# Kernel tuning notes

Hardware: AMD Instinct MI355X
Metric: run time of the kernel (lower is better)

Reference implementation:

```python
import jax, jax.numpy as jnp
import numpy as np

B, D, Q, K, C = 1024, 256, 131072, 200, 1000
TEMPERATURE = 0.07  # train-mode temperature (test=False path)
EPS = 1e-05


def setup_inputs() -> dict:
    key = jax.random.key(0)
    k1, k2, k3 = jax.random.split(key, 3)
    x = jax.random.normal(k1, (B, D), dtype=jnp.float32)
    memory = jax.random.normal(k2, (Q, D), dtype=jnp.float32)
    memory_label = jax.random.randint(k3, (Q,), 0, C, dtype=jnp.int64 if jax.config.jax_enable_x64 else jnp.int32)
    return {"x": x, "memory": memory, "memory_label": memory_label}


def reference(x, memory, memory_label):
    # dist = normalize(x) @ memory.T  -> [B, Q]
    xn = x / jnp.linalg.norm(x, axis=-1, keepdims=True)
    dist = jnp.einsum('bd,qd->bq', xn, memory)
    # top-k similarities and indices -> [B, K]
    sim_weight, sim_indices = jax.lax.top_k(dist, K)
    sim_labels = memory_label[sim_indices]  # [B, K]
    w = jax.nn.softmax(sim_weight / TEMPERATURE, axis=1)  # [B, K]
    # Fused one-hot scatter + weighted sum: scatter-add weights per class.
    rows = jnp.arange(B)[:, None]  # [B, 1] broadcast against [B, K]
    pred_scores = jnp.zeros((B, C), dtype=w.dtype).at[rows, sim_labels].add(w)
    return jnp.minimum(pred_scores + EPS, 1.0)
```

## Files before the change

### kernel.cpp

```cpp
#include <hip/hip_runtime.h>
#include <hip/hip_bf16.h>
#include <hip/hip_fp16.h>

#define B_ 1024
#define D_ 256
#define Q_ 131072
#define K_ 200
#define C_ 1000
#define INV_T 14.285714285714286f
#define EPS_ 1e-5f
#define CAP 2048
#define T0S 43.2f

#define TBM 128
#define NSL 16
#define HCAP 1024
#define FT 512

typedef __attribute__((ext_vector_type(2))) long lng2;
typedef __attribute__((ext_vector_type(4))) float f32x4;

__device__ __forceinline__ unsigned key_of(float v) {
    unsigned u = __float_as_uint(v);
    return (u & 0x80000000u) ? ~u : (u | 0x80000000u);
}
__device__ __forceinline__ int binof(float v) {
    int b = (int)(key_of(v) >> 16) - 0xC000;
    return b < 0 ? 0 : (b > 255 ? 255 : b);
}
__device__ __forceinline__ unsigned pk4(float a, float b, float c, float d) {
    int u = __builtin_amdgcn_cvt_pk_fp8_f32(a, b, 0, false);
    u = __builtin_amdgcn_cvt_pk_fp8_f32(c, d, u, true);
    return (unsigned)u;
}

#define MFMA_FP8 __builtin_amdgcn_mfma_f32_16x16x32_fp8_fp8

__global__ __launch_bounds__(256) void normsplit_kernel(const float* __restrict__ x,
                                                        float* __restrict__ xn,
                                                        unsigned char* __restrict__ af8,
                                                        unsigned* __restrict__ cnt) {
    int row = blockIdx.x, tid = threadIdx.x;
    if (tid == 0) cnt[row] = 0u;
    float v = x[row * D_ + tid];
    float s = v * v;
#pragma unroll
    for (int off = 32; off > 0; off >>= 1) s += __shfl_xor(s, off);
    __shared__ float wsum[4];
    int lane = tid & 63, wid = tid >> 6;
    if (lane == 0) wsum[wid] = s;
    __syncthreads();
    float tot = wsum[0] + wsum[1] + wsum[2] + wsum[3];
    float xv = v / sqrtf(tot);
    xn[row * D_ + tid] = xv;
    int t = tid >> 5, kb = (tid >> 3) & 3, j = tid & 7;
    int p = __builtin_amdgcn_cvt_pk_fp8_f32(xv * 16.f, 0.f, 0, false);
    af8[row * 256 + kb * 64 + t * 8 + j] = (unsigned char)(p & 0xFF);
}

__global__ __launch_bounds__(256) void convB_kernel(const float* __restrict__ m,
                                                    uint4* __restrict__ bf8,
                                                    __half* __restrict__ mh) {
    const int NCH = Q_ * D_ / 16;
    for (int g = blockIdx.x * 256 + threadIdx.x; g < NCH; g += gridDim.x * 256) {
        int panel = g >> 9, o = g & 511;
        int P = o >> 7, r = o & 127, ch = r >> 6, w = r & 63, kb = w >> 4, c = w & 15;
        int q = panel * 32 + ch * 16 + c;
        const float* src = m + (size_t)q * D_ + P * 64 + kb * 8;
        float4 f0 = *(const float4*)(src);
        float4 f1 = *(const float4*)(src + 4);
        float4 g0 = *(const float4*)(src + 32);
        float4 g1 = *(const float4*)(src + 36);
        uint4 ov;
        ov.x = pk4(f0.x, f0.y, f0.z, f0.w);
        ov.y = pk4(f1.x, f1.y, f1.z, f1.w);
        ov.z = pk4(g0.x, g0.y, g0.z, g0.w);
        ov.w = pk4(g1.x, g1.y, g1.z, g1.w);
        bf8[g] = ov;
        __half* mhp = mh + (size_t)q * D_ + P * 64 + kb * 8;
        __half2 ph[4];
        ph[0] = __floats2half2_rn(f0.x, f0.y); ph[1] = __floats2half2_rn(f0.z, f0.w);
        ph[2] = __floats2half2_rn(f1.x, f1.y); ph[3] = __floats2half2_rn(f1.z, f1.w);
        *(uint4*)mhp = *(const uint4*)ph;
        ph[0] = __floats2half2_rn(g0.x, g0.y); ph[1] = __floats2half2_rn(g0.z, g0.w);
        ph[2] = __floats2half2_rn(g1.x, g1.y); ph[3] = __floats2half2_rn(g1.z, g1.w);
        *(uint4*)(mhp + 32) = *(const uint4*)ph;
    }
}

__global__ __launch_bounds__(512, 4) void mfma_gemm_filter(const unsigned char* __restrict__ Af8,
                                                           const unsigned char* __restrict__ Bf8,
                                                           unsigned* __restrict__ candi,
                                                           unsigned* __restrict__ cnt) {
    __shared__ unsigned hits[HCAP];
    __shared__ unsigned hcnt;

    const int tid = threadIdx.x;
    const int lane = tid & 63, wid = tid >> 6;
    const int wr = wid >> 2, wn = wid & 3;
    const int l15 = lane & 15, kb = lane >> 4;

    const int l = blockIdx.x;
    const int logical = (l & 7) * 128 + (l >> 3);
    const int cg = logical >> 3;
    const int band = logical & 7;
    const int arow0 = band * TBM;

    if (tid == 0) hcnt = 0u;
    __syncthreads();

    long a[4][8];
#pragma unroll
    for (int m = 0; m < 4; ++m) {
        const unsigned char* ab = Af8 + (size_t)(arow0 + wr * 64 + m * 16 + l15) * 256 + kb * 64;
#pragma unroll
        for (int t2 = 0; t2 < 4; ++t2) {
            lng2 v = *(const lng2*)(ab + t2 * 16);
            a[m][2 * t2] = v.x;
            a[m][2 * t2 + 1] = v.y;
        }
    }

    const unsigned char* Bwave = Bf8 + (size_t)cg * 262144 + (wn >> 1) * 8192
                               + (wn & 1) * 1024 + (((kb << 4) + l15) << 4) + 4096;
    const unsigned char* pA = Bwave;
    const unsigned char* pB = Bwave + 16384;
#define LDBo(PTR, P_) (*(const lng2*)((PTR) + ((P_) * 2048 - 4096)))
#define LOADSL(BUF, PTR) do {                                                  \
    BUF[0] = LDBo(PTR, 0); BUF[1] = LDBo(PTR, 1);                              \
    BUF[2] = LDBo(PTR, 2); BUF[3] = LDBo(PTR, 3);                              \
} while (0)

    f32x4 zero4 = {0.f, 0.f, 0.f, 0.f};
    f32x4 acc[4];

#define MF4Z(AK, BV) do {                                                      \
    acc[0] = MFMA_FP8(a[0][AK], (BV), zero4, 0, 0, 0);                         \
    acc[1] = MFMA_FP8(a[1][AK], (BV), zero4, 0, 0, 0);                         \
    acc[2] = MFMA_FP8(a[2][AK], (BV), zero4, 0, 0, 0);                         \
    acc[3] = MFMA_FP8(a[3][AK], (BV), zero4, 0, 0, 0);                         \
} while (0)
#define MF4(AK, BV) do {                                                       \
    acc[0] = MFMA_FP8(a[0][AK], (BV), acc[0], 0, 0, 0);                        \
    acc[1] = MFMA_FP8(a[1][AK], (BV), acc[1], 0, 0, 0);                        \
    acc[2] = MFMA_FP8(a[2][AK], (BV), acc[2], 0, 0, 0);                        \
    acc[3] = MFMA_FP8(a[3][AK], (BV), acc[3], 0, 0, 0);                        \
} while (0)
#define COMPSL(BUF) do {                                                       \
    __builtin_amdgcn_s_setprio(1);                                             \
    MF4Z(0, BUF[0].x); MF4(1, BUF[0].y);                                       \
    MF4(2, BUF[1].x);  MF4(3, BUF[1].y);                                       \
    MF4(4, BUF[2].x);  MF4(5, BUF[2].y);                                       \
    MF4(6, BUF[3].x);  MF4(7, BUF[3].y);                                       \
    __builtin_amdgcn_s_setprio(0);                                             \
} while (0)

#define FILTER(I_) do {                                                        \
    float mx0 = fmaxf(fmaxf(acc[0][0], acc[0][1]), fmaxf(acc[0][2], acc[0][3])); \
    float mx1 = fmaxf(fmaxf(acc[1][0], acc[1][1]), fmaxf(acc[1][2], acc[1][3])); \
    float mx2 = fmaxf(fmaxf(acc[2][0], acc[2][1]), fmaxf(acc[2][2], acc[2][3])); \
    float mx3 = fmaxf(fmaxf(acc[3][0], acc[3][1]), fmaxf(acc[3][2], acc[3][3])); \
    if (fmaxf(fmaxf(mx0, mx1), fmaxf(mx2, mx3)) > T0S) {                       \
        const unsigned gc_ = (unsigned)(cg * 1024 + (wn + 4 * (I_)) * 16 + l15); \
        _Pragma("unroll")                                                      \
        for (int m = 0; m < 4; ++m)                                            \
            _Pragma("unroll")                                                  \
            for (int r = 0; r < 4; ++r)                                        \
                if (acc[m][r] > T0S) {                                         \
                    unsigned lr_ = (unsigned)(wr * 64 + m * 16 + kb * 4 + r);  \
                    unsigned p_ = atomicAdd(&hcnt, 1u);                        \
                    if (p_ < HCAP) hits[p_] = (lr_ << 17) | gc_;               \
                }                                                              \
    }                                                                          \
} while (0)

    lng2 bufA[4], bufB[4];
    LOADSL(bufA, pA);
#pragma unroll 1
    for (int i2 = 0; i2 < NSL; i2 += 2) {
        LOADSL(bufB, pB);
        pB += 32768;
        COMPSL(bufA);
        FILTER(i2);
        if (i2 + 2 < NSL) { pA += 32768; LOADSL(bufA, pA); }
        COMPSL(bufB);
        FILTER(i2 + 1);
    }

    __syncthreads();
    const unsigned nh = (hcnt < (unsigned)HCAP) ? hcnt : (unsigned)HCAP;
    for (unsigned i = tid; i < nh; i += 512) {
        unsigned e = hits[i];
        int grow = band * TBM + (int)(e >> 17);
        unsigned gcol = e & 0x1FFFFu;
        unsigned pos = atomicAdd(&cnt[grow], 1u);
        if (pos < CAP) candi[(long long)grow * CAP + pos] = gcol;
    }
#undef LDBo
#undef LOADSL
#undef MF4Z
#undef MF4
#undef COMPSL
#undef FILTER
}

__global__ __launch_bounds__(FT) void final_kernel(const unsigned* __restrict__ cnt,
                                                   const unsigned* __restrict__ candi,
                                                   const float* __restrict__ xn,
                                                   const __half* __restrict__ mh,
                                                   const int* __restrict__ labels,
                                                   float* __restrict__ out) {
    __shared__ float cval[CAP];
    __shared__ unsigned cidx[CAP];
    __shared__ unsigned char incl[CAP];
    __shared__ float xs[D_];
    __shared__ float bins[C_];
    __shared__ float segf[FT];
    __shared__ unsigned hist[256];
    __shared__ float binval[256];
    __shared__ int binpos[256];
    __shared__ int sh_bstar, sh_g0, sh_m;

    const int tid = threadIdx.x;
    const int row = blockIdx.x;
    unsigned c = cnt[row];
    const int n = (c < (unsigned)CAP) ? (int)c : CAP;

    if (tid < D_) xs[tid] = xn[row * D_ + tid];
    for (int i = tid; i < C_; i += FT) bins[i] = 0.f;
    if (tid < 256) hist[tid] = 0u;
    if (tid == 0) sh_m = 0;
    for (int i = tid; i < n; i += FT) cidx[i] = candi[(long long)row * CAP + i];
    __syncthreads();

    for (int i = tid; i < n; i += FT) {
        const uint4* mrow = (const uint4*)(mh + (size_t)cidx[i] * D_);
        float s = 0.f;
#pragma unroll 8
        for (int k = 0; k < 32; ++k) {
            uint4 mv = mrow[k];
            const __half2* hp = (const __half2*)&mv;
            float2 f0 = __half22float2(hp[0]);
            float2 f1 = __half22float2(hp[1]);
            float2 f2 = __half22float2(hp[2]);
            float2 f3 = __half22float2(hp[3]);
            const float* xp = xs + k * 8;
            s += f0.x * xp[0] + f0.y * xp[1] + f1.x * xp[2] + f1.y * xp[3]
               + f2.x * xp[4] + f2.y * xp[5] + f3.x * xp[6] + f3.y * xp[7];
        }
        cval[i] = s;
    }
    __syncthreads();

    float lm = -3.4e38f;
    for (int i = tid; i < n; i += FT) lm = fmaxf(lm, cval[i]);
    segf[tid] = lm;
    __syncthreads();
    for (int off = FT / 2; off > 0; off >>= 1) {
        if (tid < off) segf[tid] = fmaxf(segf[tid], segf[tid + off]);
        __syncthreads();
    }
    const float m = segf[0];
    __syncthreads();

    if (n > K_) {
        for (int i = tid; i < n; i += FT) atomicAdd(&hist[binof(cval[i])], 1u);
        __syncthreads();
        if (tid == 0) {
            unsigned cum = 0; int b = 255;
            for (; b >= 0; --b) { cum += hist[b]; if (cum >= (unsigned)K_) break; }
            sh_bstar = b;
            sh_g0 = (int)(cum - hist[b]);
        }
        __syncthreads();
        const int bst = sh_bstar;
        for (int i = tid; i < n; i += FT) {
            int hb = binof(cval[i]);
            incl[i] = (hb > bst) ? (unsigned char)1 : (unsigned char)0;
            if (hb == bst) {
                int p = atomicAdd(&sh_m, 1);
                if (p < 256) { binval[p] = cval[i]; binpos[p] = i; }
            }
        }
        __syncthreads();
        const int m2 = (sh_m < 256) ? sh_m : 256;
        const int rem = K_ - sh_g0;
        for (int e = tid; e < m2; e += FT) {
            unsigned ke = key_of(binval[e]);
            int g = 0;
            for (int j = 0; j < m2; ++j) {
                unsigned kj = key_of(binval[j]);
                g += (kj > ke) || (kj == ke && j < e);
            }
            incl[binpos[e]] = (g < rem) ? (unsigned char)1 : (unsigned char)0;
        }
        __syncthreads();
    } else {
        for (int i = tid; i < n; i += FT) incl[i] = 1;
        __syncthreads();
    }

    float part = 0.f;
    for (int i = tid; i < n; i += FT) {
        float e = incl[i] ? __expf((cval[i] - m) * INV_T) : 0.f;
        cval[i] = e;
        part += e;
    }
    segf[tid] = part;
    __syncthreads();
    for (int off = FT / 2; off > 0; off >>= 1) {
        if (tid < off) segf[tid] += segf[tid + off];
        __syncthreads();
    }
    const float invS = 1.f / segf[0];

    for (int i = tid; i < n; i += FT) {
        float e = cval[i];
        if (e > 0.f) {
            int lbl = labels[cidx[i]];
            if ((unsigned)lbl < (unsigned)C_) atomicAdd(&bins[lbl], e);
        }
    }
    __syncthreads();

    const long long ob = (long long)row * C_;
    for (int i = tid; i < C_; i += FT)
        out[ob + i] = fminf(bins[i] * invS + EPS_, 1.0f);
}

extern "C" void kernel_launch(void* const* d_in, const int* in_sizes, int n_in,
                              void* d_out, int out_size, void* d_ws, size_t ws_size,
                              hipStream_t stream) {
    const float* x = (const float*)d_in[0];
    const float* mem = (const float*)d_in[1];
    const int* lab = (const int*)d_in[2];
    float* out = (float*)d_out;

    float* xn = (float*)d_ws;
    unsigned char* Af8 = (unsigned char*)(xn + (size_t)B_ * D_);
    unsigned char* Bf8 = Af8 + (size_t)B_ * D_;
    __half* mh = (__half*)(Bf8 + (size_t)Q_ * D_);
    unsigned* candi = (unsigned*)(mh + (size_t)Q_ * D_);
    unsigned* cnt = candi + (size_t)B_ * CAP;

    normsplit_kernel<<<B_, 256, 0, stream>>>(x, xn, Af8, cnt);
    convB_kernel<<<4096, 256, 0, stream>>>(mem, (uint4*)Bf8, mh);
    mfma_gemm_filter<<<(B_ / TBM) * (Q_ / (NSL * 4 * 16)), 512, 0, stream>>>(Af8, Bf8, candi, cnt);
    final_kernel<<<B_, FT, 0, stream>>>(cnt, candi, xn, mh, lab, out);
}
```

Measured before the change: 193.1 us.

## Switch filter GEMM to scaled 16x16x128 FP8 MFMA with matching operand layout

Replaces the 16x16x32 FP8 MFMA chain (8 per tile column) with the gfx950 scaled 16x16x128 f8f6f4 MFMA (2 per tile column), using unit scales. To feed the wider K-per-lane operands, the fp8 packing of both the normalized query and the memory bank is relaid out into 32-byte contiguous chunks per lane. This cuts MFMA instruction count and issue overhead, but operands are now 8-int vectors, so register pressure rises, and the occupancy hint drops from 4 to 3 waves.

New measurement: 208.9 us. 1.08x slower.

```diff
diff --git a/kernel.cpp b/kernel.cpp
--- a/kernel.cpp
+++ b/kernel.cpp
@@ -17,7 +17,7 @@
 #define HCAP 1024
 #define FT 512
 
-typedef __attribute__((ext_vector_type(2))) long lng2;
+typedef __attribute__((ext_vector_type(8))) int i32x8;
 typedef __attribute__((ext_vector_type(4))) float f32x4;
 
 __device__ __forceinline__ unsigned key_of(float v) {
@@ -34,7 +34,8 @@
     return (unsigned)u;
 }
 
-#define MFMA_FP8 __builtin_amdgcn_mfma_f32_16x16x32_fp8_fp8
+#define SMFMA(A_, B_, C_) __builtin_amdgcn_mfma_scale_f32_16x16x128_f8f6f4( \
+    (A_), (B_), (C_), 0, 0, 0, 0x7F7F7F7F, 0, 0x7F7F7F7F)
 
 __global__ __launch_bounds__(256) void normsplit_kernel(const float* __restrict__ x,
                                                         float* __restrict__ xn,
@@ -53,9 +54,8 @@
     float tot = wsum[0] + wsum[1] + wsum[2] + wsum[3];
     float xv = v / sqrtf(tot);
     xn[row * D_ + tid] = xv;
-    int t = tid >> 5, kb = (tid >> 3) & 3, j = tid & 7;
     int p = __builtin_amdgcn_cvt_pk_fp8_f32(xv * 16.f, 0.f, 0, false);
-    af8[row * 256 + kb * 64 + t * 8 + j] = (unsigned char)(p & 0xFF);
+    af8[row * D_ + tid] = (unsigned char)(p & 0xFF);
 }
 
 __global__ __launch_bounds__(256) void convB_kernel(const float* __restrict__ m,
@@ -63,32 +63,32 @@
                                                     __half* __restrict__ mh) {
     const int NCH = Q_ * D_ / 16;
     for (int g = blockIdx.x * 256 + threadIdx.x; g < NCH; g += gridDim.x * 256) {
-        int panel = g >> 9, o = g & 511;
-        int P = o >> 7, r = o & 127, ch = r >> 6, w = r & 63, kb = w >> 4, c = w & 15;
-        int q = panel * 32 + ch * 16 + c;
-        const float* src = m + (size_t)q * D_ + P * 64 + kb * 8;
+        int slice = g >> 8, o = g & 255;
+        int h = o >> 7, kb = (o >> 5) & 3, c = (o >> 1) & 15, hf = o & 1;
+        int q = slice * 16 + c;
+        const float* src = m + (size_t)q * D_ + h * 128 + kb * 32 + hf * 16;
         float4 f0 = *(const float4*)(src);
         float4 f1 = *(const float4*)(src + 4);
-        float4 g0 = *(const float4*)(src + 32);
-        float4 g1 = *(const float4*)(src + 36);
+        float4 f2 = *(const float4*)(src + 8);
+        float4 f3 = *(const float4*)(src + 12);
         uint4 ov;
         ov.x = pk4(f0.x, f0.y, f0.z, f0.w);
         ov.y = pk4(f1.x, f1.y, f1.z, f1.w);
-        ov.z = pk4(g0.x, g0.y, g0.z, g0.w);
-        ov.w = pk4(g1.x, g1.y, g1.z, g1.w);
+        ov.z = pk4(f2.x, f2.y, f2.z, f2.w);
+        ov.w = pk4(f3.x, f3.y, f3.z, f3.w);
         bf8[g] = ov;
-        __half* mhp = mh + (size_t)q * D_ + P * 64 + kb * 8;
+        __half* mhp = mh + (size_t)q * D_ + h * 128 + kb * 32 + hf * 16;
         __half2 ph[4];
         ph[0] = __floats2half2_rn(f0.x, f0.y); ph[1] = __floats2half2_rn(f0.z, f0.w);
         ph[2] = __floats2half2_rn(f1.x, f1.y); ph[3] = __floats2half2_rn(f1.z, f1.w);
         *(uint4*)mhp = *(const uint4*)ph;
-        ph[0] = __floats2half2_rn(g0.x, g0.y); ph[1] = __floats2half2_rn(g0.z, g0.w);
-        ph[2] = __floats2half2_rn(g1.x, g1.y); ph[3] = __floats2half2_rn(g1.z, g1.w);
-        *(uint4*)(mhp + 32) = *(const uint4*)ph;
-    }
-}
-
-__global__ __launch_bounds__(512, 4) void mfma_gemm_filter(const unsigned char* __restrict__ Af8,
+        ph[0] = __floats2half2_rn(f2.x, f2.y); ph[1] = __floats2half2_rn(f2.z, f2.w);
+        ph[2] = __floats2half2_rn(f3.x, f3.y); ph[3] = __floats2half2_rn(f3.z, f3.w);
+        *(uint4*)(mhp + 8) = *(const uint4*)ph;
+    }
+}
+
+__global__ __launch_bounds__(512, 3) void mfma_gemm_filter(const unsigned char* __restrict__ Af8,
                                                            const unsigned char* __restrict__ Bf8,
                                                            unsigned* __restrict__ candi,
                                                            unsigned* __restrict__ cnt) {
@@ -109,49 +109,46 @@
     if (tid == 0) hcnt = 0u;
     __syncthreads();
 
-    long a[4][8];
+    union U8 { i32x8 v; uint4 q[2]; };
+
+    i32x8 a[4][2];
 #pragma unroll
     for (int m = 0; m < 4; ++m) {
-        const unsigned char* ab = Af8 + (size_t)(arow0 + wr * 64 + m * 16 + l15) * 256 + kb * 64;
-#pragma unroll
-        for (int t2 = 0; t2 < 4; ++t2) {
-            lng2 v = *(const lng2*)(ab + t2 * 16);
-            a[m][2 * t2] = v.x;
-            a[m][2 * t2 + 1] = v.y;
-        }
-    }
-
-    const unsigned char* Bwave = Bf8 + (size_t)cg * 262144 + (wn >> 1) * 8192
-                               + (wn & 1) * 1024 + (((kb << 4) + l15) << 4) + 4096;
+        const unsigned char* ab = Af8 + (size_t)(arow0 + wr * 64 + m * 16 + l15) * D_ + kb * 32;
+        U8 u0, u1;
+        u0.q[0] = *(const uint4*)(ab);
+        u0.q[1] = *(const uint4*)(ab + 16);
+        u1.q[0] = *(const uint4*)(ab + 128);
+        u1.q[1] = *(const uint4*)(ab + 128 + 16);
+        a[m][0] = u0.v;
+        a[m][1] = u1.v;
+    }
+
+    const unsigned char* Bwave = Bf8 + ((size_t)cg * 64 + wn) * 4096 + kb * 512 + l15 * 32;
     const unsigned char* pA = Bwave;
     const unsigned char* pB = Bwave + 16384;
-#define LDBo(PTR, P_) (*(const lng2*)((PTR) + ((P_) * 2048 - 4096)))
 #define LOADSL(BUF, PTR) do {                                                  \
-    BUF[0] = LDBo(PTR, 0); BUF[1] = LDBo(PTR, 1);                              \
-    BUF[2] = LDBo(PTR, 2); BUF[3] = LDBo(PTR, 3);                              \
+    U8 u0_, u1_;                                                               \
+    u0_.q[0] = *(const uint4*)((PTR));                                         \
+    u0_.q[1] = *(const uint4*)((PTR) + 16);                                    \
+    u1_.q[0] = *(const uint4*)((PTR) + 2048);                                  \
+    u1_.q[1] = *(const uint4*)((PTR) + 2064);                                  \
+    BUF[0] = u0_.v; BUF[1] = u1_.v;                                            \
 } while (0)
 
     f32x4 zero4 = {0.f, 0.f, 0.f, 0.f};
     f32x4 acc[4];
 
-#define MF4Z(AK, BV) do {                                                      \
-    acc[0] = MFMA_FP8(a[0][AK], (BV), zero4, 0, 0, 0);                         \
-    acc[1] = MFMA_FP8(a[1][AK], (BV), zero4, 0, 0, 0);                         \
-    acc[2] = MFMA_FP8(a[2][AK], (BV), zero4, 0, 0, 0);                         \
-    acc[3] = MFMA_FP8(a[3][AK], (BV), zero4, 0, 0, 0);                         \
-} while (0)
-#define MF4(AK, BV) do {                                                       \
-    acc[0] = MFMA_FP8(a[0][AK], (BV), acc[0], 0, 0, 0);                        \
-    acc[1] = MFMA_FP8(a[1][AK], (BV), acc[1], 0, 0, 0);                        \
-    acc[2] = MFMA_FP8(a[2][AK], (BV), acc[2], 0, 0, 0);                        \
-    acc[3] = MFMA_FP8(a[3][AK], (BV), acc[3], 0, 0, 0);                        \
-} while (0)
 #define COMPSL(BUF) do {                                                       \
     __builtin_amdgcn_s_setprio(1);                                             \
-    MF4Z(0, BUF[0].x); MF4(1, BUF[0].y);                                       \
-    MF4(2, BUF[1].x);  MF4(3, BUF[1].y);                                       \
-    MF4(4, BUF[2].x);  MF4(5, BUF[2].y);                                       \
-    MF4(6, BUF[3].x);  MF4(7, BUF[3].y);                                       \
+    acc[0] = SMFMA(a[0][0], BUF[0], zero4);                                    \
+    acc[1] = SMFMA(a[1][0], BUF[0], zero4);                                    \
+    acc[2] = SMFMA(a[2][0], BUF[0], zero4);                                    \
+    acc[3] = SMFMA(a[3][0], BUF[0], zero4);                                    \
+    acc[0] = SMFMA(a[0][1], BUF[1], acc[0]);                                   \
+    acc[1] = SMFMA(a[1][1], BUF[1], acc[1]);                                   \
+    acc[2] = SMFMA(a[2][1], BUF[1], acc[2]);                                   \
+    acc[3] = SMFMA(a[3][1], BUF[1], acc[3]);                                   \
     __builtin_amdgcn_s_setprio(0);                                             \
 } while (0)
 
@@ -174,7 +171,7 @@
     }                                                                          \
 } while (0)
 
-    lng2 bufA[4], bufB[4];
+    i32x8 bufA[2], bufB[2];
     LOADSL(bufA, pA);
 #pragma unroll 1
     for (int i2 = 0; i2 < NSL; i2 += 2) {
@@ -196,10 +193,7 @@
         unsigned pos = atomicAdd(&cnt[grow], 1u);
         if (pos < CAP) candi[(long long)grow * CAP + pos] = gcol;
     }
-#undef LDBo
 #undef LOADSL
-#undef MF4Z
-#undef MF4
 #undef COMPSL
 #undef FILTER
 }
```
